# Optimization experiments

Hardware: AMD Instinct MI355X
Metric: run time of the kernel (lower is better)

## Reference

```python
import jax, jax.numpy as jnp
import numpy as np

WCD, WCOV, WQUAL = 1.0, 1e-4, 1e-4
BIG = 1e10  # penalty to exclude zero-rows from min/argmin


def _calus(x, y):
    # x: [B, N, 3], y: [B, M, 3]
    B, N, _ = x.shape
    M = y.shape[1]
    # _remove_zero_rows filters rows whose coordinate SUM is zero -> mask instead
    mx = x.sum(-1) != 0  # [B, N] valid x points
    my = y.sum(-1) != 0  # [B, M] valid y points
    dt = x.dtype
    # squared pairwise distances d[b, j, i] = ||x[b,i] - y[b,j]||^2  (expanded form)
    xn = jnp.sum(x * x, axis=-1)  # [B, N]
    yn = jnp.sum(y * y, axis=-1)  # [B, M]
    d = yn[:, :, None] + xn[:, None, :] - 2.0 * jnp.einsum('bmc,bnc->bmn', y, x)  # [B, M, N]
    # push invalid rows/cols out of every min
    d = d + jnp.where(mx, 0.0, BIG).astype(dt)[:, None, :] \
          + jnp.where(my, 0.0, BIG).astype(dt)[:, :, None]
    x_min = jnp.min(d, axis=1)     # [B, N] nearest-y distance per x point
    x_arg = jnp.argmin(d, axis=1)  # [B, N] index into y
    y_min = jnp.min(d, axis=2)     # [B, M] nearest-x distance per y point
    y_arg = jnp.argmin(d, axis=2)  # [B, M] index into x
    fmx, fmy = mx.astype(dt), my.astype(dt)
    nx, ny = fmx.sum(-1), fmy.sum(-1)  # valid counts per sample
    # chamfer = mean over x-points + mean over y-points (torch cat+sum)
    cd = jnp.sum(x_min * fmx, -1) / nx + jnp.sum(y_min * fmy, -1) / ny  # [B]
    # coverage: fraction of y indices hit by some valid x point (unique count)
    rows = jnp.arange(B)[:, None]
    hit_y = jnp.zeros((B, M), dt).at[rows, x_arg].max(fmx)
    cov = hit_y.sum(-1) / ny  # [B]
    # quality: fraction of x indices hit by some valid y point
    hit_x = jnp.zeros((B, N), dt).at[rows, y_arg].max(fmy)
    qual = hit_x.sum(-1) / nx  # [B]
    return cd.mean(), cov.mean(), qual.mean()


def setup_inputs() -> dict:
    key = jax.random.key(0)
    kx, ky = jax.random.split(key)
    B, N, M = 32, 2048, 2048
    x = jax.random.normal(kx, (B, N, 3), dtype=jnp.float32)
    y = jax.random.normal(ky, (B, M, 3), dtype=jnp.float32)
    return {"x": x, "y": y}


def reference(x, y):
    cd, cov, qual = _calus(x, y)
    val = WCD * cd - WCOV * cov - WQUAL * qual
    return (val, cd, cov, qual)
```

## Files before the change

### kernel.cpp

```cpp
#include <hip/hip_runtime.h>
#include <stdint.h>


#define BB 32
#define NP 2048
#define BIGF 1e10f

typedef unsigned int u32;
typedef float f2 __attribute__((ext_vector_type(2)));

#define EMB(d, jg) __uint_as_float((__float_as_uint(d) & 0xFFFFF800u) | (jg))

__device__ __forceinline__ f2 pk_fma(f2 a, f2 b, f2 c) {
  f2 d;
  asm("v_pk_fma_f32 %0, %1, %2, %3" : "=v"(d) : "v"(a), "v"(b), "v"(c));
  return d;
}
__device__ __forceinline__ float min3(float a, float b, float c) {
  float r;
  asm("v_min3_f32 %0, %1, %2, %3" : "=v"(r) : "v"(a), "v"(b), "v"(c));
  return r;
}

__global__ __launch_bounds__(512) __attribute__((amdgpu_waves_per_eu(4, 4)))
void nn_fused_kernel(const float* __restrict__ x, const float* __restrict__ y,
                     u32* __restrict__ hitpart, float* __restrict__ sums_part,
                     float* __restrict__ cnts_part) {
  int bid = blockIdx.x;
  int side = bid >> 8;
  int b = (bid >> 3) & 31;
  int pc = bid & 7;
  int tid = threadIdx.x;
  int w = __builtin_amdgcn_readfirstlane(tid >> 6);
  int lane = tid & 63;

  __shared__ float4 qs[2048];
  __shared__ u32 merged[8][256];
  __shared__ float pws[256];
  __shared__ u32 hitlds[64];
  __shared__ float redc[4], redn[4];

  {
    const float* qraw = (side ? x : y) + b * NP * 3 + tid * 12;
    float4 f0 = *(const float4*)(qraw);
    float4 f1 = *(const float4*)(qraw + 4);
    float4 g2 = *(const float4*)(qraw + 8);
    float n0 = f0.x * f0.x + f0.y * f0.y + f0.z * f0.z;
    float n1 = f0.w * f0.w + f1.x * f1.x + f1.y * f1.y;
    float n2 = f1.z * f1.z + f1.w * f1.w + g2.x * g2.x;
    float n3 = g2.y * g2.y + g2.z * g2.z + g2.w * g2.w;
    if (f0.x + f0.y + f0.z == 0.f) n0 += BIGF;
    if (f0.w + f1.x + f1.y == 0.f) n1 += BIGF;
    if (f1.z + f1.w + g2.x == 0.f) n2 += BIGF;
    if (g2.y + g2.z + g2.w == 0.f) n3 += BIGF;
    qs[4 * tid + 0] = make_float4(f0.x, f0.w, f0.y, f1.x);
    qs[4 * tid + 1] = make_float4(f0.z, f1.y, n0, n1);
    qs[4 * tid + 2] = make_float4(f1.z, g2.y, f1.w, g2.z);
    qs[4 * tid + 3] = make_float4(g2.x, g2.w, n2, n3);
  }

  const float* praw = (side ? y : x) + (b * NP + pc * 256) * 3;
  f2 pmx[4], pmy[4], pmz[4];
  float best[4];
#pragma unroll
  for (int k = 0; k < 4; ++k) {
    int pl = lane + 64 * k;
    float p0 = praw[3 * pl], p1 = praw[3 * pl + 1], p2 = praw[3 * pl + 2];
    pmx[k] = (f2){-2.f * p0, -2.f * p0};
    pmy[k] = (f2){-2.f * p1, -2.f * p1};
    pmz[k] = (f2){-2.f * p2, -2.f * p2};
    if (w == 0) {
      float pn = p0 * p0 + p1 * p1 + p2 * p2;
      if (p0 + p1 + p2 == 0.f) pn += BIGF;
      pws[pl] = pn;
    }
    best[k] = 3.0e38f;
  }
  if (tid < 64) hitlds[tid] = 0u;
  __syncthreads();

  const float4* qr = &qs[w * 256];
  u32 je = (u32)(w * 256);
#pragma unroll 8
  for (int r = 0; r < 128; ++r) {
    float4 A = qr[2 * r];
    float4 B = qr[2 * r + 1];
    f2 qx2 = (f2){A.x, A.y};
    f2 qy2 = (f2){A.z, A.w};
    f2 qz2 = (f2){B.x, B.y};
    f2 qw2 = (f2){B.z, B.w};
    u32 jg = je + 2 * (u32)r, jg1 = jg + 1;
#pragma unroll
    for (int k = 0; k < 4; ++k) {
      f2 d2 = pk_fma(qx2, pmx[k], pk_fma(qy2, pmy[k], pk_fma(qz2, pmz[k], qw2)));
      best[k] = min3(best[k], EMB(d2.x, jg), EMB(d2.y, jg1));
    }
  }

  merged[w][lane +   0] = __float_as_uint(best[0]);
  merged[w][lane +  64] = __float_as_uint(best[1]);
  merged[w][lane + 128] = __float_as_uint(best[2]);
  merged[w][lane + 192] = __float_as_uint(best[3]);
  __syncthreads();

  float contrib = 0.f, cnt = 0.f;
  if (tid < 256) {
    float bd = __uint_as_float(merged[0][tid]);
#pragma unroll
    for (int ww = 1; ww < 8; ++ww) bd = fminf(bd, __uint_as_float(merged[ww][tid]));
    u32 bits = __float_as_uint(bd);
    u32 bi = bits & 0x7FFu;
    float dmin = __uint_as_float(bits & 0xFFFFF800u);
    float pwv = pws[tid];
    bool valid = (pwv < 1e9f);
    contrib = valid ? (dmin + pwv) : 0.f;
    cnt = valid ? 1.f : 0.f;
    if (valid) atomicOr(&hitlds[bi >> 5], 1u << (bi & 31));
  }
  for (int o = 32; o > 0; o >>= 1) {
    contrib += __shfl_down(contrib, o, 64);
    cnt += __shfl_down(cnt, o, 64);
  }
  if (tid < 256 && lane == 0) { redc[w] = contrib; redn[w] = cnt; }
  __syncthreads();
  if (tid == 0) {
    sums_part[bid] = redc[0] + redc[1] + redc[2] + redc[3];
    cnts_part[bid] = redn[0] + redn[1] + redn[2] + redn[3];
  }
  if (tid < 64) hitpart[bid * 64 + tid] = hitlds[tid];
}

__global__ __launch_bounds__(512) void assemble_kernel(const u32* __restrict__ hitpart,
                                                       const float* __restrict__ sums_part,
                                                       const float* __restrict__ cnts_part,
                                                       float* __restrict__ out) {
  __shared__ float hs[64], ss[64], cs[64];
  int tid = threadIdx.x;
  int sb = tid >> 3, c = tid & 7;
  float h = 0.f;
  for (int wd = c; wd < 64; wd += 8) {
    u32 m = 0u;
#pragma unroll
    for (int blk = 0; blk < 8; ++blk) m |= hitpart[(sb * 8 + blk) * 64 + wd];
    h += (float)__popc(m);
  }
  h += __shfl_down(h, 4, 8);
  h += __shfl_down(h, 2, 8);
  h += __shfl_down(h, 1, 8);
  if (c == 0) {
    float s = 0.f, n = 0.f;
#pragma unroll
    for (int blk = 0; blk < 8; ++blk) {
      s += sums_part[sb * 8 + blk];
      n += cnts_part[sb * 8 + blk];
    }
    hs[sb] = h; ss[sb] = s; cs[sb] = n;
  }
  __syncthreads();
  if (tid < 64) {
    float cd = 0.f, cov = 0.f, qual = 0.f;
    if (tid < BB) {
      float nx = cs[tid], ny = cs[BB + tid];
      cd = ss[tid] / nx + ss[BB + tid] / ny;
      cov = hs[tid] / ny;
      qual = hs[BB + tid] / nx;
    }
    for (int o = 32; o > 0; o >>= 1) {
      cd += __shfl_down(cd, o, 64);
      cov += __shfl_down(cov, o, 64);
      qual += __shfl_down(qual, o, 64);
    }
    if (tid == 0) {
      cd /= (float)BB; cov /= (float)BB; qual /= (float)BB;
      out[0] = cd - 1e-4f * cov - 1e-4f * qual;
      out[1] = cd;
      out[2] = cov;
      out[3] = qual;
    }
  }
}

extern "C" void kernel_launch(void* const* d_in, const int* in_sizes, int n_in,
                              void* d_out, int out_size, void* d_ws, size_t ws_size,
                              hipStream_t stream) {
  const float* x = (const float*)d_in[0];
  const float* y = (const float*)d_in[1];
  float* out = (float*)d_out;
  char* ws = (char*)d_ws;

  u32* hitpart = (u32*)ws;
  float* sums_part = (float*)(ws + 131072);
  float* cnts_part = (float*)(ws + 133120);

  nn_fused_kernel<<<512, 512, 0, stream>>>(x, y, hitpart, sums_part, cnts_part);
  assemble_kernel<<<1, 512, 0, stream>>>(hitpart, sums_part, cnts_part, out);
}
```

Baseline: 92.31 us.

## Split query range across two blocks and merge partial minima in new kernel

The nearest-neighbor kernel now splits each batch's query set into two halves, launching 1024 blocks instead of 512. Each block writes its packed distance+index minima to a workspace buffer. A new merge kernel combines the two halves and computes the chamfer sums, counts and hit bitmasks. The aim is more parallelism and occupancy (launch_bounds 512,8, half the LDS), at the cost of an extra kernel launch and a global round trip for the partial minima.

```diff
diff --git a/kernel.cpp b/kernel.cpp
--- a/kernel.cpp
+++ b/kernel.cpp
@@ -22,41 +22,34 @@
   return r;
 }
 
-__global__ __launch_bounds__(512) __attribute__((amdgpu_waves_per_eu(4, 4)))
-void nn_fused_kernel(const float* __restrict__ x, const float* __restrict__ y,
-                     u32* __restrict__ hitpart, float* __restrict__ sums_part,
-                     float* __restrict__ cnts_part) {
+__global__ __launch_bounds__(512, 8) void nn_kernel(const float* __restrict__ x,
+                                                    const float* __restrict__ y,
+                                                    u32* __restrict__ part) {
   int bid = blockIdx.x;
-  int side = bid >> 8;
-  int b = (bid >> 3) & 31;
-  int pc = bid & 7;
+  int side = bid >> 9;
+  int b = (bid >> 4) & 31;
+  int pc = (bid >> 1) & 7;
+  int qc = bid & 1;
   int tid = threadIdx.x;
   int w = __builtin_amdgcn_readfirstlane(tid >> 6);
   int lane = tid & 63;
 
-  __shared__ float4 qs[2048];
+  __shared__ float4 qs[1024];
   __shared__ u32 merged[8][256];
-  __shared__ float pws[256];
-  __shared__ u32 hitlds[64];
-  __shared__ float redc[4], redn[4];
 
   {
-    const float* qraw = (side ? x : y) + b * NP * 3 + tid * 12;
-    float4 f0 = *(const float4*)(qraw);
-    float4 f1 = *(const float4*)(qraw + 4);
-    float4 g2 = *(const float4*)(qraw + 8);
-    float n0 = f0.x * f0.x + f0.y * f0.y + f0.z * f0.z;
-    float n1 = f0.w * f0.w + f1.x * f1.x + f1.y * f1.y;
-    float n2 = f1.z * f1.z + f1.w * f1.w + g2.x * g2.x;
-    float n3 = g2.y * g2.y + g2.z * g2.z + g2.w * g2.w;
-    if (f0.x + f0.y + f0.z == 0.f) n0 += BIGF;
-    if (f0.w + f1.x + f1.y == 0.f) n1 += BIGF;
-    if (f1.z + f1.w + g2.x == 0.f) n2 += BIGF;
-    if (g2.y + g2.z + g2.w == 0.f) n3 += BIGF;
-    qs[4 * tid + 0] = make_float4(f0.x, f0.w, f0.y, f1.x);
-    qs[4 * tid + 1] = make_float4(f0.z, f1.y, n0, n1);
-    qs[4 * tid + 2] = make_float4(f1.z, g2.y, f1.w, g2.z);
-    qs[4 * tid + 3] = make_float4(g2.x, g2.w, n2, n3);
+    const float* qraw = (side ? x : y) + (b * NP + qc * 1024) * 3 + tid * 6;
+    f2 a01 = *(const f2*)(qraw);
+    f2 a23 = *(const f2*)(qraw + 2);
+    f2 a45 = *(const f2*)(qraw + 4);
+    float q0x = a01.x, q0y = a01.y, q0z = a23.x;
+    float q1x = a23.y, q1y = a45.x, q1z = a45.y;
+    float n0 = q0x * q0x + q0y * q0y + q0z * q0z;
+    float n1 = q1x * q1x + q1y * q1y + q1z * q1z;
+    if (q0x + q0y + q0z == 0.f) n0 += BIGF;
+    if (q1x + q1y + q1z == 0.f) n1 += BIGF;
+    qs[2 * tid]     = make_float4(q0x, q1x, q0y, q1y);
+    qs[2 * tid + 1] = make_float4(q0z, q1z, n0, n1);
   }
 
   const float* praw = (side ? y : x) + (b * NP + pc * 256) * 3;
@@ -69,20 +62,14 @@
     pmx[k] = (f2){-2.f * p0, -2.f * p0};
     pmy[k] = (f2){-2.f * p1, -2.f * p1};
     pmz[k] = (f2){-2.f * p2, -2.f * p2};
-    if (w == 0) {
-      float pn = p0 * p0 + p1 * p1 + p2 * p2;
-      if (p0 + p1 + p2 == 0.f) pn += BIGF;
-      pws[pl] = pn;
-    }
     best[k] = 3.0e38f;
   }
-  if (tid < 64) hitlds[tid] = 0u;
-  __syncthreads();
-
-  const float4* qr = &qs[w * 256];
-  u32 je = (u32)(w * 256);
+  __syncthreads();
+
+  const float4* qr = &qs[w * 128];
+  u32 je = (u32)(qc * 1024 + w * 128);
 #pragma unroll 8
-  for (int r = 0; r < 128; ++r) {
+  for (int r = 0; r < 64; ++r) {
     float4 A = qr[2 * r];
     float4 B = qr[2 * r + 1];
     f2 qx2 = (f2){A.x, A.y};
@@ -103,25 +90,49 @@
   merged[w][lane + 192] = __float_as_uint(best[3]);
   __syncthreads();
 
-  float contrib = 0.f, cnt = 0.f;
   if (tid < 256) {
     float bd = __uint_as_float(merged[0][tid]);
 #pragma unroll
     for (int ww = 1; ww < 8; ++ww) bd = fminf(bd, __uint_as_float(merged[ww][tid]));
-    u32 bits = __float_as_uint(bd);
-    u32 bi = bits & 0x7FFu;
-    float dmin = __uint_as_float(bits & 0xFFFFF800u);
-    float pwv = pws[tid];
-    bool valid = (pwv < 1e9f);
-    contrib = valid ? (dmin + pwv) : 0.f;
-    cnt = valid ? 1.f : 0.f;
-    if (valid) atomicOr(&hitlds[bi >> 5], 1u << (bi & 31));
-  }
+    part[qc * 131072 + side * 65536 + b * 2048 + pc * 256 + tid] = __float_as_uint(bd);
+  }
+}
+
+__global__ __launch_bounds__(256) void merge_kernel(const float* __restrict__ x,
+                                                    const float* __restrict__ y,
+                                                    const u32* __restrict__ part,
+                                                    u32* __restrict__ hitpart,
+                                                    float* __restrict__ sums_part,
+                                                    float* __restrict__ cnts_part) {
+  int bid = blockIdx.x;
+  int side = bid >> 8;
+  int b = (bid >> 3) & 31;
+  int pc = bid & 7;
+  int tid = threadIdx.x;
+  int lane = tid & 63, w = tid >> 6;
+
+  __shared__ u32 hitlds[64];
+  __shared__ float redc[4], redn[4];
+  if (tid < 64) hitlds[tid] = 0u;
+  __syncthreads();
+
+  int pidx = side * 65536 + b * 2048 + pc * 256 + tid;
+  float bd = fminf(__uint_as_float(part[pidx]), __uint_as_float(part[131072 + pidx]));
+  u32 bits = __float_as_uint(bd);
+  u32 bi = bits & 0x7FFu;
+  float dmin = __uint_as_float(bits & 0xFFFFF800u);
+  const float* praw = (side ? y : x) + (b * NP + pc * 256 + tid) * 3;
+  float p0 = praw[0], p1 = praw[1], p2 = praw[2];
+  bool valid = (p0 + p1 + p2) != 0.f;
+  float contrib = valid ? (dmin + p0 * p0 + p1 * p1 + p2 * p2) : 0.f;
+  float cnt = valid ? 1.f : 0.f;
+  if (valid) atomicOr(&hitlds[bi >> 5], 1u << (bi & 31));
+
   for (int o = 32; o > 0; o >>= 1) {
     contrib += __shfl_down(contrib, o, 64);
     cnt += __shfl_down(cnt, o, 64);
   }
-  if (tid < 256 && lane == 0) { redc[w] = contrib; redn[w] = cnt; }
+  if (lane == 0) { redc[w] = contrib; redn[w] = cnt; }
   __syncthreads();
   if (tid == 0) {
     sums_part[bid] = redc[0] + redc[1] + redc[2] + redc[3];
@@ -191,7 +202,9 @@
   u32* hitpart = (u32*)ws;
   float* sums_part = (float*)(ws + 131072);
   float* cnts_part = (float*)(ws + 133120);
-
-  nn_fused_kernel<<<512, 512, 0, stream>>>(x, y, hitpart, sums_part, cnts_part);
+  u32* part = (u32*)(ws + 135168);
+
+  nn_kernel<<<1024, 512, 0, stream>>>(x, y, part);
+  merge_kernel<<<512, 256, 0, stream>>>(x, y, part, hitpart, sums_part, cnts_part);
   assemble_kernel<<<1, 512, 0, stream>>>(hitpart, sums_part, cnts_part, out);
 }
```

New measurement: 90.73 us, median of 2. No clear change (-1.7%).
